# Kernel optimization log

Measured on AMD Instinct MI355X. Metric: run time of the kernel, lower is better.

The kernel has to match this reference:

```python
import jax, jax.numpy as jnp
import numpy as np

H = 1024
E = 8
TOP_K = 2


def setup_inputs() -> dict:
    key = jax.random.key(0)
    ks = jax.random.split(key, 6)
    B, S = 4, 2048
    hidden_states = jax.random.normal(ks[0], (B, S, H), dtype=jnp.float32)
    # router weight, init N(0, 0.02)
    router_w = jax.random.normal(ks[1], (E, H), dtype=jnp.float32) * 0.02
    # stacked expert FFN params (nn.Linear: y = x @ W.T + b)
    lim = 1.0 / np.sqrt(H)
    W1 = jax.random.uniform(ks[2], (E, H, H), minval=-lim, maxval=lim, dtype=jnp.float32)
    b1 = jax.random.uniform(ks[3], (E, H), minval=-lim, maxval=lim, dtype=jnp.float32)
    W2 = jax.random.uniform(ks[4], (E, H, H), minval=-lim, maxval=lim, dtype=jnp.float32)
    b2 = jax.random.uniform(ks[5], (E, H), minval=-lim, maxval=lim, dtype=jnp.float32)
    return {"hidden_states": hidden_states, "router_w": router_w,
            "W1": W1, "b1": b1, "W2": W2, "b2": b2}


def reference(hidden_states, router_w, W1, b1, W2, b2):
    B, S, _ = hidden_states.shape
    # ---- router ----
    logits = jnp.einsum('bsh,eh->bse', hidden_states, router_w)  # [B,S,E]
    router_probs = jax.nn.softmax(logits.astype(jnp.float32), axis=-1)
    top_vals, top_idx = jax.lax.top_k(router_probs, TOP_K)        # [B,S,K]
    top_vals = top_vals / jnp.sum(top_vals, axis=-1, keepdims=True)  # norm_topk_prob
    # per-token per-expert combine weight (sum of top-k weights matching expert)
    w = jnp.sum(jax.nn.one_hot(top_idx, E, dtype=top_vals.dtype) * top_vals[..., None], axis=-2)  # [B,S,E]
    # ---- dense all-expert FFN (faithful to reference: every expert on every token) ----
    h1 = jax.nn.relu(jnp.einsum('bsh,efh->bsef', hidden_states, W1) + b1)   # [B,S,E,F]
    expert_out = jnp.einsum('bsef,egf->bseg', h1, W2) + b2                  # [B,S,E,H]
    moe_out = jnp.einsum('bseh,bse->bsh', expert_out, w)
    return hidden_states + moe_out, router_probs
```

## Files before the change

kernel.cpp:

```cpp
#include <hip/hip_runtime.h>
#include <hip/hip_bf16.h>


#define HD   1024
#define NTOK 8192
#define NEXP 8
#define BM   128
#define BN   128
#define BK   32
#define ZROW 8192
#define MAXP 17408
#define EP_LDSW 136

typedef __attribute__((ext_vector_type(8))) short  vshort8;
typedef __attribute__((ext_vector_type(4))) short  vshort4;
typedef __attribute__((ext_vector_type(4))) float  vfloat4;

typedef __attribute__((address_space(1))) const unsigned gas_uint;
typedef __attribute__((address_space(3))) unsigned       las_uint;

__device__ __forceinline__ void gld16(const void* g, void* l) {
    __builtin_amdgcn_global_load_lds((gas_uint*)g, (las_uint*)l, 16, 0, 0);
}

__device__ __forceinline__ short bf16r(float f) {
    union { float f; unsigned u; } a; a.f = f;
    unsigned r = a.u + 0x7FFFu + ((a.u >> 16) & 1u);
    return (short)(r >> 16);
}

__global__ void init_kernel(int* counts, int* fill, int* pair_token) {
    int i = blockIdx.x * 256 + threadIdx.x;
    if (i < NEXP) { counts[i] = 0; fill[i] = 0; }
    if (i < MAXP) pair_token[i] = ZROW;
}

__global__ __launch_bounds__(256) void router_kernel(
    const float* __restrict__ x, const float* __restrict__ rw,
    float* __restrict__ out,
    float* __restrict__ probs_out, int2* __restrict__ tok_top,
    float2* __restrict__ tok_w, int* __restrict__ counts) {
    __shared__ float rws[NEXP * HD];
    __shared__ int hist[NEXP];
    int t = threadIdx.x;
    if (t < NEXP) hist[t] = 0;
    for (int j = 0; j < 8; ++j) {
        int idx = j * 1024 + t * 4;
        *(vfloat4*)(rws + idx) = *(const vfloat4*)(rw + idx);
    }
    __syncthreads();
    int wave = t >> 6, lane = t & 63;
    for (int it = 0; it < 8; ++it) {
        int token = blockIdx.x * 32 + it * 4 + wave;
        const float* xr = x + (size_t)token * HD;
        float part[NEXP];
#pragma unroll
        for (int e = 0; e < NEXP; ++e) part[e] = 0.f;
        for (int j = 0; j < 4; ++j) {
            int off = j * 256 + lane * 4;
            vfloat4 xv = *(const vfloat4*)(xr + off);
            *(vfloat4*)(out + (size_t)token * HD + off) = xv;
#pragma unroll
            for (int e = 0; e < NEXP; ++e) {
                vfloat4 wv = *(const vfloat4*)(rws + e * HD + off);
                part[e] += xv.x * wv.x + xv.y * wv.y + xv.z * wv.z + xv.w * wv.w;
            }
        }
#pragma unroll
        for (int e = 0; e < NEXP; ++e)
            for (int off = 32; off; off >>= 1)
                part[e] += __shfl_xor(part[e], off, 64);
        if (lane == 0) {
            float m = part[0];
#pragma unroll
            for (int e = 1; e < NEXP; ++e) m = fmaxf(m, part[e]);
            float p[NEXP], s = 0.f;
#pragma unroll
            for (int e = 0; e < NEXP; ++e) { p[e] = expf(part[e] - m); s += p[e]; }
            float inv = 1.f / s;
#pragma unroll
            for (int e = 0; e < NEXP; ++e) {
                p[e] *= inv;
                probs_out[(size_t)token * NEXP + e] = p[e];
            }
            int i0 = 0;
#pragma unroll
            for (int e = 1; e < NEXP; ++e) if (p[e] > p[i0]) i0 = e;
            int i1 = (i0 == 0) ? 1 : 0;
#pragma unroll
            for (int e = 0; e < NEXP; ++e) if (e != i0 && p[e] > p[i1]) i1 = e;
            float s2 = 1.f / (p[i0] + p[i1]);
            tok_top[token] = make_int2(i0, i1);
            tok_w[token]   = make_float2(p[i0] * s2, p[i1] * s2);
            atomicAdd(&hist[i0], 1);
            atomicAdd(&hist[i1], 1);
        }
    }
    __syncthreads();
    if (t < NEXP) atomicAdd(&counts[t], hist[t]);
}

__global__ __launch_bounds__(256) void scatter_kernel(
    const int2* __restrict__ tok_top, const float2* __restrict__ tok_w,
    const int* __restrict__ counts, int* fill,
    int* __restrict__ pair_token, float* __restrict__ pair_w) {
    __shared__ int lhist[NEXP];
    __shared__ int lbase[NEXP];
    int t = threadIdx.x;
    if (t < NEXP) lhist[t] = 0;
    __syncthreads();
    int offs[NEXP];
    {
        int acc = 0;
#pragma unroll
        for (int f = 0; f < NEXP; ++f) {
            offs[f] = acc;
            acc += (counts[f] + 127) & ~127;
        }
    }
    int token = blockIdx.x * 256 + t;
    int2 ti = tok_top[token];
    float2 tw = tok_w[token];
    int r0 = atomicAdd(&lhist[ti.x], 1);
    int r1 = atomicAdd(&lhist[ti.y], 1);
    __syncthreads();
    if (t < NEXP) lbase[t] = atomicAdd(&fill[t], lhist[t]);
    __syncthreads();
    int s0 = offs[ti.x] + lbase[ti.x] + r0;
    pair_token[s0] = token; pair_w[s0] = tw.x;
    int s1 = offs[ti.y] + lbase[ti.y] + r1;
    pair_token[s1] = token; pair_w[s1] = tw.y;
}

__global__ void convw_kernel(const float* __restrict__ W1, const float* __restrict__ W2,
                             short* __restrict__ D1, short* __restrict__ D2) {
    size_t t = (size_t)blockIdx.x * 256 + threadIdx.x;
    const size_t PER = (size_t)NEXP * HD * HD / 8;
    const float* src = W1; short* dst = D1;
    if (t >= PER) { t -= PER; src = W2; dst = D2; }
    size_t C = t >> 6;
    int l  = (int)(t & 63);
    int kc = (int)(C & 31);
    int ng = (int)((C >> 5) & 63);
    int ei = (int)(C >> 11);
    int n = ng * 16 + (l & 15);
    int k = kc * 32 + (l >> 4) * 8;
    const float* s = src + ((size_t)ei * HD + n) * HD + k;
    vfloat4 a = *(const vfloat4*)s;
    vfloat4 b = *(const vfloat4*)(s + 4);
    vshort8 o;
    o[0] = bf16r(a.x); o[1] = bf16r(a.y); o[2] = bf16r(a.z); o[3] = bf16r(a.w);
    o[4] = bf16r(b.x); o[5] = bf16r(b.y); o[6] = bf16r(b.z); o[7] = bf16r(b.w);
    *(vshort8*)(dst + t * 8) = o;
}

__global__ __launch_bounds__(256) void gather_kernel(
    const float* __restrict__ x, const int* __restrict__ pair_token,
    short* __restrict__ xg) {
    int id = blockIdx.x * 256 + threadIdx.x;
    int C = id >> 6, l = id & 63;
    int slot = ((C >> 5) << 4) + (l & 15);
    int k = (C & 31) * 32 + (l >> 4) * 8;
    int tok = pair_token[slot];
    vshort8 o = {0, 0, 0, 0, 0, 0, 0, 0};
    if (tok < ZROW) {
        const float* s = x + (size_t)tok * HD + k;
        vfloat4 a = *(const vfloat4*)s;
        vfloat4 b = *(const vfloat4*)(s + 4);
        o[0] = bf16r(a.x); o[1] = bf16r(a.y); o[2] = bf16r(a.z); o[3] = bf16r(a.w);
        o[4] = bf16r(b.x); o[5] = bf16r(b.y); o[6] = bf16r(b.z); o[7] = bf16r(b.w);
    }
    *(vshort8*)(xg + (size_t)id * 8) = o;
}

template <int MODE>
__global__ __launch_bounds__(256, 3) void moe_gemm(
    const short* __restrict__ A, const short* __restrict__ Bw,
    const float* __restrict__ bias, const int* __restrict__ pair_token,
    const float* __restrict__ pair_w, const int* __restrict__ counts,
    short* __restrict__ h1sw_out, float* __restrict__ out) {
    __shared__ short smem[16384];

    const int row0 = blockIdx.x * BM;
    int e = 0;
    {
        int csum = 0;
#pragma unroll
        for (int f = 0; f < NEXP; ++f) {
            int p = (counts[f] + 127) & ~127;
            if (csum + p <= row0) e = f + 1;
            csum += p;
        }
        if (row0 >= csum) return;
    }

    const int t = threadIdx.x;
    const int wave = t >> 6, lane = t & 63;
    const int wm = wave >> 1, wn = wave & 1;
    const int quad = lane >> 4, l16 = lane & 15;
    const int colb = blockIdx.y * BN;

    const char* agp0 = (const char*)A +
        ((size_t)(row0 >> 4) + 2 * wave) * 32768 + lane * 16;
    const char* agp1 = agp0 + 32768;
    const char* bgp0 = (const char*)Bw +
        ((size_t)e * 64 + (colb >> 4) + 2 * wave) * 32768 + lane * 16;
    const char* bgp1 = bgp0 + 32768;

    vfloat4 acc[4][4];
#pragma unroll
    for (int i = 0; i < 4; ++i)
#pragma unroll
        for (int j = 0; j < 4; ++j)
            acc[i][j] = (vfloat4){0.f, 0.f, 0.f, 0.f};

#define STAGE(bsel, kt_)                                                      \
    {                                                                         \
        short* sa_ = smem + (bsel) * 4096;                                    \
        short* sb_ = smem + 8192 + (bsel) * 4096;                             \
        gld16(agp0 + (size_t)(kt_) * 1024, sa_ + (2 * wave) * 512);           \
        gld16(agp1 + (size_t)(kt_) * 1024, sa_ + (2 * wave + 1) * 512);       \
        gld16(bgp0 + (size_t)(kt_) * 1024, sb_ + (2 * wave) * 512);           \
        gld16(bgp1 + (size_t)(kt_) * 1024, sb_ + (2 * wave + 1) * 512);       \
    }

    STAGE(0, 0)
    int cur = 0;
    for (int kt = 0; kt < HD / BK; ++kt) {
        if (kt < HD / BK - 1) {
            STAGE(cur ^ 1, kt + 1)
            asm volatile("s_waitcnt vmcnt(4)" ::: "memory");
        } else {
            asm volatile("s_waitcnt vmcnt(0)" ::: "memory");
        }
        __builtin_amdgcn_s_barrier();
        asm volatile("" ::: "memory");
        const short* sa = smem + cur * 4096;
        const short* sb = smem + 8192 + cur * 4096;
        vshort8 af[4], bfr[4];
#pragma unroll
        for (int i = 0; i < 4; ++i)
            af[i] = *(const vshort8*)(sa + (wm * 4 + i) * 512 + lane * 8);
#pragma unroll
        for (int j = 0; j < 4; ++j)
            bfr[j] = *(const vshort8*)(sb + (wn * 4 + j) * 512 + lane * 8);
#pragma unroll
        for (int i = 0; i < 4; ++i)
#pragma unroll
            for (int j = 0; j < 4; ++j)
                acc[i][j] = __builtin_amdgcn_mfma_f32_16x16x32_bf16(af[i], bfr[j], acc[i][j], 0, 0, 0);
        asm volatile("" ::: "memory");
        __builtin_amdgcn_s_barrier();
        cur ^= 1;
    }
#undef STAGE

    if (MODE == 0) {
        __syncthreads();
#pragma unroll
        for (int p = 0; p < 2; ++p) {
            if (wm == p) {
#pragma unroll
                for (int j = 0; j < 4; ++j) {
                    int col = wn * 64 + j * 16 + l16;
                    float bv = bias[e * HD + colb + col];
#pragma unroll
                    for (int i = 0; i < 4; ++i) {
                        int rl = i * 16 + quad * 4;
#pragma unroll
                        for (int reg = 0; reg < 4; ++reg) {
                            float v = acc[i][j][reg] + bv;
                            v = v > 0.f ? v : 0.f;
                            smem[(rl + reg) * EP_LDSW + col] = bf16r(v);
                        }
                    }
                }
            }
            __syncthreads();
#pragma unroll
            for (int c = 0; c < 4; ++c) {
                int idx = wave * 4 + c;
                int rg = idx >> 2, kc = idx & 3;
                vshort8 v = *(const vshort8*)(smem + (rg * 16 + l16) * EP_LDSW + kc * 32 + quad * 8);
                size_t chunk = ((size_t)(row0 >> 4) + p * 4 + rg) * 32 + (colb >> 5) + kc;
                *(vshort8*)(h1sw_out + chunk * 512 + lane * 8) = v;
            }
            if (p == 0) __syncthreads();
        }
    } else {
        int tok[4][4]; float wv[4][4];
#pragma unroll
        for (int i = 0; i < 4; ++i)
#pragma unroll
            for (int reg = 0; reg < 4; ++reg) {
                int r = row0 + wm * 64 + i * 16 + quad * 4 + reg;
                tok[i][reg] = pair_token[r];
                wv[i][reg] = pair_w[r];
            }
#pragma unroll
        for (int j = 0; j < 4; ++j) {
            int col = colb + wn * 64 + j * 16 + l16;
            float bv = bias[e * HD + col];
#pragma unroll
            for (int i = 0; i < 4; ++i)
#pragma unroll
                for (int reg = 0; reg < 4; ++reg)
                    if (tok[i][reg] < ZROW)
                        atomicAdd(out + (size_t)tok[i][reg] * HD + col,
                                  wv[i][reg] * (acc[i][j][reg] + bv));
        }
    }
}

extern "C" void kernel_launch(void* const* d_in, const int* in_sizes, int n_in,
                              void* d_out, int out_size, void* d_ws, size_t ws_size,
                              hipStream_t stream) {
    const float* x  = (const float*)d_in[0];
    const float* rw = (const float*)d_in[1];
    const float* W1 = (const float*)d_in[2];
    const float* b1 = (const float*)d_in[3];
    const float* W2 = (const float*)d_in[4];
    const float* b2 = (const float*)d_in[5];
    float* out   = (float*)d_out;
    float* probs = out + (size_t)NTOK * HD;

    char* ws = (char*)d_ws;
    short* xg = (short*)ws;            ws += (size_t)MAXP * HD * 2;
    short* h1 = (short*)ws;            ws += (size_t)MAXP * HD * 2;
    int*   pair_token = (int*)ws;      ws += MAXP * 4;
    float* pair_w     = (float*)ws;    ws += MAXP * 4;
    int*   counts = (int*)ws;          ws += 256;
    int*   fill   = (int*)ws;          ws += 256;
    int2*   tok_top = (int2*)ws;       ws += NTOK * 8;
    float2* tok_w   = (float2*)ws;     ws += NTOK * 8;
    short* w1sw = (short*)ws;          ws += (size_t)NEXP * HD * HD * 2;
    short* w2sw = (short*)ws;          ws += (size_t)NEXP * HD * HD * 2;
    (void)ws_size;

    init_kernel<<<MAXP / 256, 256, 0, stream>>>(counts, fill, pair_token);
    router_kernel<<<NTOK / 32, 256, 0, stream>>>(x, rw, out, probs,
                                                 tok_top, tok_w, counts);
    scatter_kernel<<<NTOK / 256, 256, 0, stream>>>(tok_top, tok_w, counts, fill,
                                                   pair_token, pair_w);
    int cg = (int)(2 * ((size_t)NEXP * HD * HD / 8) / 256);
    convw_kernel<<<cg, 256, 0, stream>>>(W1, W2, w1sw, w2sw);
    gather_kernel<<<(MAXP * HD / 8) / 256, 256, 0, stream>>>(x, pair_token, xg);
    dim3 gg(MAXP / BM, HD / BN);
    moe_gemm<0><<<gg, 256, 0, stream>>>(xg, w1sw, b1, pair_token, pair_w, counts, h1, nullptr);
    moe_gemm<1><<<gg, 256, 0, stream>>>(h1, w2sw, b2, pair_token, pair_w, counts, nullptr, out);
}
```

Baseline: 339.7 us.

## Enlarge MoE GEMM tiles to 256x256 with 512 threads and 4-stage pipeline

Moves the grouped expert GEMMs from 128x128 tiles with 256 threads and double buffering to 256x256 tiles with 512 threads. Four waves handle A loads and four handle B loads into a 4-deep LDS ring with prefetch distance 2. The change also raises MFMA priority with s_setprio, swizzles block order for L2 locality, and pads expert segments to 256 rows. The aim is more data reuse per loaded byte and better load/compute overlap. The cost is 128KB of LDS per block, lower occupancy, and more padded rows per expert.

```diff
diff --git a/kernel.cpp b/kernel.cpp
--- a/kernel.cpp
+++ b/kernel.cpp
@@ -5,12 +5,9 @@
 #define HD   1024
 #define NTOK 8192
 #define NEXP 8
-#define BM   128
-#define BN   128
-#define BK   32
 #define ZROW 8192
-#define MAXP 17408
-#define EP_LDSW 136
+#define MAXP 18432
+#define EPW  264
 
 typedef __attribute__((ext_vector_type(8))) short  vshort8;
 typedef __attribute__((ext_vector_type(4))) short  vshort4;
@@ -115,7 +112,7 @@
 #pragma unroll
         for (int f = 0; f < NEXP; ++f) {
             offs[f] = acc;
-            acc += (counts[f] + 127) & ~127;
+            acc += (counts[f] + 255) & ~255;
         }
     }
     int token = blockIdx.x * 256 + t;
@@ -174,20 +171,24 @@
 }
 
 template <int MODE>
-__global__ __launch_bounds__(256, 3) void moe_gemm(
+__global__ __launch_bounds__(512, 2) void moe_gemm(
     const short* __restrict__ A, const short* __restrict__ Bw,
     const float* __restrict__ bias, const int* __restrict__ pair_token,
     const float* __restrict__ pair_w, const int* __restrict__ counts,
     short* __restrict__ h1sw_out, float* __restrict__ out) {
-    __shared__ short smem[16384];
-
-    const int row0 = blockIdx.x * BM;
+    __shared__ short smem[65536];
+
+    int lin = blockIdx.y * 72 + blockIdx.x;
+    int swz = (lin & 7) * 36 + (lin >> 3);
+    int row_t = swz % 72, col_t = swz / 72;
+
+    const int row0 = row_t * 256;
     int e = 0;
     {
         int csum = 0;
 #pragma unroll
         for (int f = 0; f < NEXP; ++f) {
-            int p = (counts[f] + 127) & ~127;
+            int p = (counts[f] + 255) & ~255;
             if (csum + p <= row0) e = f + 1;
             csum += p;
         }
@@ -196,67 +197,80 @@
 
     const int t = threadIdx.x;
     const int wave = t >> 6, lane = t & 63;
-    const int wm = wave >> 1, wn = wave & 1;
+    const int wm = wave >> 2, wn = wave & 3;
     const int quad = lane >> 4, l16 = lane & 15;
-    const int colb = blockIdx.y * BN;
-
-    const char* agp0 = (const char*)A +
-        ((size_t)(row0 >> 4) + 2 * wave) * 32768 + lane * 16;
-    const char* agp1 = agp0 + 32768;
-    const char* bgp0 = (const char*)Bw +
-        ((size_t)e * 64 + (colb >> 4) + 2 * wave) * 32768 + lane * 16;
-    const char* bgp1 = bgp0 + 32768;
-
-    vfloat4 acc[4][4];
-#pragma unroll
-    for (int i = 0; i < 4; ++i)
+    const int colb = col_t * 256;
+
+    const char *sp0, *sp1, *sp2, *sp3;
+    int dof0, dof1, dof2, dof3;
+    if (wave < 4) {
+        int rgb = wave * 4;
+        const char* ab = (const char*)A + ((size_t)(row0 >> 4) + rgb) * 32768 + lane * 16;
+        sp0 = ab; sp1 = ab + 32768; sp2 = ab + 65536; sp3 = ab + 98304;
+        dof0 = (rgb + 0) * 512; dof1 = (rgb + 1) * 512;
+        dof2 = (rgb + 2) * 512; dof3 = (rgb + 3) * 512;
+    } else {
+        int cgb = (wave - 4) * 4;
+        const char* bb = (const char*)Bw +
+            ((size_t)e * 64 + (colb >> 4) + cgb) * 32768 + lane * 16;
+        sp0 = bb; sp1 = bb + 32768; sp2 = bb + 65536; sp3 = bb + 98304;
+        dof0 = 8192 + (cgb + 0) * 512; dof1 = 8192 + (cgb + 1) * 512;
+        dof2 = 8192 + (cgb + 2) * 512; dof3 = 8192 + (cgb + 3) * 512;
+    }
+
+    vfloat4 acc[8][4];
+#pragma unroll
+    for (int i = 0; i < 8; ++i)
 #pragma unroll
         for (int j = 0; j < 4; ++j)
             acc[i][j] = (vfloat4){0.f, 0.f, 0.f, 0.f};
 
-#define STAGE(bsel, kt_)                                                      \
+#define STG(P)                                                                \
     {                                                                         \
-        short* sa_ = smem + (bsel) * 4096;                                    \
-        short* sb_ = smem + 8192 + (bsel) * 4096;                             \
-        gld16(agp0 + (size_t)(kt_) * 1024, sa_ + (2 * wave) * 512);           \
-        gld16(agp1 + (size_t)(kt_) * 1024, sa_ + (2 * wave + 1) * 512);       \
-        gld16(bgp0 + (size_t)(kt_) * 1024, sb_ + (2 * wave) * 512);           \
-        gld16(bgp1 + (size_t)(kt_) * 1024, sb_ + (2 * wave + 1) * 512);       \
-    }
-
-    STAGE(0, 0)
-    int cur = 0;
-    for (int kt = 0; kt < HD / BK; ++kt) {
-        if (kt < HD / BK - 1) {
-            STAGE(cur ^ 1, kt + 1)
-            asm volatile("s_waitcnt vmcnt(4)" ::: "memory");
-        } else {
-            asm volatile("s_waitcnt vmcnt(0)" ::: "memory");
-        }
-        __builtin_amdgcn_s_barrier();
-        asm volatile("" ::: "memory");
-        const short* sa = smem + cur * 4096;
-        const short* sb = smem + 8192 + cur * 4096;
-        vshort8 af[4], bfr[4];
-#pragma unroll
-        for (int i = 0; i < 4; ++i)
-            af[i] = *(const vshort8*)(sa + (wm * 4 + i) * 512 + lane * 8);
-#pragma unroll
-        for (int j = 0; j < 4; ++j)
-            bfr[j] = *(const vshort8*)(sb + (wn * 4 + j) * 512 + lane * 8);
-#pragma unroll
-        for (int i = 0; i < 4; ++i)
-#pragma unroll
-            for (int j = 0; j < 4; ++j)
-                acc[i][j] = __builtin_amdgcn_mfma_f32_16x16x32_bf16(af[i], bfr[j], acc[i][j], 0, 0, 0);
-        asm volatile("" ::: "memory");
-        __builtin_amdgcn_s_barrier();
-        cur ^= 1;
-    }
-#undef STAGE
+        short* d_ = smem + ((P) & 3) * 16384;                                 \
+        gld16(sp0 + (size_t)(P) * 1024, d_ + dof0);                           \
+        gld16(sp1 + (size_t)(P) * 1024, d_ + dof1);                           \
+        gld16(sp2 + (size_t)(P) * 1024, d_ + dof2);                           \
+        gld16(sp3 + (size_t)(P) * 1024, d_ + dof3);                           \
+    }
+
+#define PHASE(P)                                                              \
+    {                                                                         \
+        const short* sl_ = smem + ((P) & 3) * 16384;                          \
+        vshort8 bf[4], af[8];                                                 \
+        _Pragma("unroll")                                                     \
+        for (int j = 0; j < 4; ++j)                                           \
+            bf[j] = *(const vshort8*)(sl_ + 8192 + (wn * 4 + j) * 512 + lane * 8); \
+        _Pragma("unroll")                                                     \
+        for (int i = 0; i < 8; ++i)                                           \
+            af[i] = *(const vshort8*)(sl_ + (wm * 8 + i) * 512 + lane * 8);   \
+        if ((P) < 30) STG((P) + 2)                                            \
+        __builtin_amdgcn_s_setprio(1);                                        \
+        _Pragma("unroll")                                                     \
+        for (int i = 0; i < 8; ++i)                                           \
+            _Pragma("unroll")                                                 \
+            for (int j = 0; j < 4; ++j)                                       \
+                acc[i][j] = __builtin_amdgcn_mfma_f32_16x16x32_bf16(          \
+                    af[i], bf[j], acc[i][j], 0, 0, 0);                        \
+        __builtin_amdgcn_s_setprio(0);                                        \
+        if ((P) < 30) { asm volatile("s_waitcnt vmcnt(4)" ::: "memory"); }    \
+        else          { asm volatile("s_waitcnt vmcnt(0)" ::: "memory"); }    \
+        __builtin_amdgcn_s_barrier();                                         \
+    }
+
+    STG(0)
+    STG(1)
+    asm volatile("s_waitcnt vmcnt(4)" ::: "memory");
+    __builtin_amdgcn_s_barrier();
+
+#pragma unroll
+    for (int P = 0; P < 30; ++P) PHASE(P)
+    PHASE(30)
+    PHASE(31)
+#undef PHASE
+#undef STG
 
     if (MODE == 0) {
-        __syncthreads();
 #pragma unroll
         for (int p = 0; p < 2; ++p) {
             if (wm == p) {
@@ -265,49 +279,43 @@
                     int col = wn * 64 + j * 16 + l16;
                     float bv = bias[e * HD + colb + col];
 #pragma unroll
-                    for (int i = 0; i < 4; ++i) {
+                    for (int i = 0; i < 8; ++i) {
                         int rl = i * 16 + quad * 4;
 #pragma unroll
                         for (int reg = 0; reg < 4; ++reg) {
                             float v = acc[i][j][reg] + bv;
                             v = v > 0.f ? v : 0.f;
-                            smem[(rl + reg) * EP_LDSW + col] = bf16r(v);
+                            smem[(rl + reg) * EPW + col] = bf16r(v);
                         }
                     }
                 }
             }
             __syncthreads();
 #pragma unroll
-            for (int c = 0; c < 4; ++c) {
-                int idx = wave * 4 + c;
-                int rg = idx >> 2, kc = idx & 3;
-                vshort8 v = *(const vshort8*)(smem + (rg * 16 + l16) * EP_LDSW + kc * 32 + quad * 8);
-                size_t chunk = ((size_t)(row0 >> 4) + p * 4 + rg) * 32 + (colb >> 5) + kc;
+            for (int kc = 0; kc < 8; ++kc) {
+                vshort8 v = *(const vshort8*)(smem + (wave * 16 + l16) * EPW + kc * 32 + quad * 8);
+                size_t chunk = ((size_t)(row0 >> 4) + p * 8 + wave) * 32 + (colb >> 5) + kc;
                 *(vshort8*)(h1sw_out + chunk * 512 + lane * 8) = v;
             }
             if (p == 0) __syncthreads();
         }
     } else {
-        int tok[4][4]; float wv[4][4];
-#pragma unroll
-        for (int i = 0; i < 4; ++i)
-#pragma unroll
-            for (int reg = 0; reg < 4; ++reg) {
-                int r = row0 + wm * 64 + i * 16 + quad * 4 + reg;
-                tok[i][reg] = pair_token[r];
-                wv[i][reg] = pair_w[r];
-            }
-#pragma unroll
-        for (int j = 0; j < 4; ++j) {
-            int col = colb + wn * 64 + j * 16 + l16;
-            float bv = bias[e * HD + col];
-#pragma unroll
-            for (int i = 0; i < 4; ++i)
-#pragma unroll
-                for (int reg = 0; reg < 4; ++reg)
-                    if (tok[i][reg] < ZROW)
-                        atomicAdd(out + (size_t)tok[i][reg] * HD + col,
-                                  wv[i][reg] * (acc[i][j][reg] + bv));
+#pragma unroll
+        for (int i = 0; i < 8; ++i) {
+            int rbase = row0 + wm * 128 + i * 16 + quad * 4;
+            int   tok0 = pair_token[rbase + 0], tok1 = pair_token[rbase + 1];
+            int   tok2 = pair_token[rbase + 2], tok3 = pair_token[rbase + 3];
+            float wv0 = pair_w[rbase + 0], wv1 = pair_w[rbase + 1];
+            float wv2 = pair_w[rbase + 2], wv3 = pair_w[rbase + 3];
+#pragma unroll
+            for (int j = 0; j < 4; ++j) {
+                int col = colb + wn * 64 + j * 16 + l16;
+                float bv = bias[e * HD + col];
+                if (tok0 < ZROW) atomicAdd(out + (size_t)tok0 * HD + col, wv0 * (acc[i][j][0] + bv));
+                if (tok1 < ZROW) atomicAdd(out + (size_t)tok1 * HD + col, wv1 * (acc[i][j][1] + bv));
+                if (tok2 < ZROW) atomicAdd(out + (size_t)tok2 * HD + col, wv2 * (acc[i][j][2] + bv));
+                if (tok3 < ZROW) atomicAdd(out + (size_t)tok3 * HD + col, wv3 * (acc[i][j][3] + bv));
+            }
         }
     }
 }
@@ -344,8 +352,8 @@
                                                    pair_token, pair_w);
     int cg = (int)(2 * ((size_t)NEXP * HD * HD / 8) / 256);
     convw_kernel<<<cg, 256, 0, stream>>>(W1, W2, w1sw, w2sw);
-    gather_kernel<<<(MAXP * HD / 8) / 256, 256, 0, stream>>>(x, pair_token, xg);
-    dim3 gg(MAXP / BM, HD / BN);
-    moe_gemm<0><<<gg, 256, 0, stream>>>(xg, w1sw, b1, pair_token, pair_w, counts, h1, nullptr);
-    moe_gemm<1><<<gg, 256, 0, stream>>>(h1, w2sw, b2, pair_token, pair_w, counts, nullptr, out);
-}
+    gather_kernel<<<(MAXP * (HD / 8)) / 256, 256, 0, stream>>>(x, pair_token, xg);
+    dim3 gg(72, 4);
+    moe_gemm<0><<<gg, 512, 0, stream>>>(xg, w1sw, b1, pair_token, pair_w, counts, h1, nullptr);
+    moe_gemm<1><<<gg, 512, 0, stream>>>(h1, w2sw, b2, pair_token, pair_w, counts, nullptr, out);
+}
```

Measured after the change: 375.4 us. 10.5% more time.
